# Optimization experiments

Hardware: AMD Instinct MI355X
Metric: run time of the kernel (lower is better)

The kernel has to match this reference:

```python
import jax, jax.numpy as jnp
import numpy as np

B, H, W, D, U = 32, 64, 64, 256, 512


def setup_inputs() -> dict:
    key = jax.random.key(0)
    k1, k2, k3, k4, k5 = jax.random.split(key, 5)
    he_in = np.sqrt(2.0 / D)
    he_u = np.sqrt(2.0 / U)
    return {
        "x": jax.random.normal(k1, (B, H, W, D), dtype=jnp.float32),
        "wax": jax.random.normal(k2, (D, U), dtype=jnp.float32) * he_in,
        "w0": jax.random.normal(k3, (U, U), dtype=jnp.float32) * he_u,
        "w1": jax.random.normal(k4, (U, U), dtype=jnp.float32) * he_u,
        "ba": jax.random.normal(k5, (1, U), dtype=jnp.float32) * 0.01,
    }


def reference(x, wax, w0, w1, ba):
    """2D MDRNN, direction (+1,+1), zero initial state, tanh activation.

    h[i,j] = tanh(x[i,j] @ wax + h[i-1,j] @ w0 + h[i,j-1] @ w1 + ba)
    (out-of-bound neighbors contribute zero, matching the original with
    zero initial state). Returns h at final position (H-1, W-1): (B, U).
    """
    b, h, w, d = x.shape
    u = wax.shape[1]
    # Precompute input contribution for the whole grid: (H, W, B, U)
    zx = jnp.einsum("bhwd,du->hwbu", x, wax) + ba

    def row_step(prev_row, zx_row):
        # prev_row: (W, B, U) = h[i-1, :]; zx_row: (W, B, U)
        pre = zx_row + jnp.einsum("wbu,uv->wbv", prev_row, w0)

        def col_step(h_left, pre_j):
            h_ij = jnp.tanh(pre_j + h_left @ w1)
            return h_ij, h_ij

        _, row = jax.lax.scan(col_step, jnp.zeros((b, u), x.dtype), pre)
        return row, None

    last_row, _ = jax.lax.scan(row_step, jnp.zeros((w, b, u), x.dtype), zx)
    return last_row[-1]  # (B, U)
```

## Files before the change

### kernel.cpp

```cpp
#include <hip/hip_runtime.h>
#include <stdint.h>

#define H_ 64
#define W_ 64
#define D_ 256
#define U_ 512
#define KREC 1024
#define CELL_ELT (32 * U_)

typedef __attribute__((ext_vector_type(8))) _Float16 half8;
typedef __attribute__((ext_vector_type(8))) unsigned short ushort8;
typedef __attribute__((ext_vector_type(4))) float f32x4;

__device__ __forceinline__ unsigned short f2h(float f) {
    _Float16 h = (_Float16)f;
    return __builtin_bit_cast(unsigned short, h);
}

__device__ __forceinline__ int swzo(int r, int o) {
    return o ^ (((r ^ (o >> 7)) & 7) << 4);
}

__device__ __forceinline__ void llc_load2(const int* p0, const int* p1, int& a, int& b) {
    asm volatile("global_load_dword %0, %2, off sc0 sc1\n\t"
                 "global_load_dword %1, %3, off sc0 sc1\n\t"
                 "s_waitcnt vmcnt(0)"
                 : "=v"(a), "=v"(b) : "v"(p0), "v"(p1) : "memory");
}

__global__ void prep_w(const float* __restrict__ w0,
                       const float* __restrict__ w1,
                       unsigned short* __restrict__ wcT2) {
    int n = blockIdx.x;
    for (int k = threadIdx.x; k < KREC; k += blockDim.x) {
        float v = (k < U_) ? w0[(size_t)k * U_ + n] : w1[(size_t)(k - U_) * U_ + n];
        wcT2[(size_t)n * KREC + k] = f2h(v);
    }
}

__global__ void prep_waxT(const float* __restrict__ wax,
                          unsigned short* __restrict__ waxT) {
    int n = blockIdx.x;
    for (int k = threadIdx.x; k < D_; k += blockDim.x)
        waxT[(size_t)n * D_ + k] = f2h(wax[(size_t)k * U_ + n]);
}

__global__ __launch_bounds__(256) void prep_z(
    const float* __restrict__ x,
    const unsigned short* __restrict__ waxT,
    const float* __restrict__ ba,
    float* __restrict__ zfb)
{
    __shared__ char xs[32 * 512];
    const int cell = blockIdx.x;
    const int t = threadIdx.x, lane = t & 63, wv = t >> 6;
    const int l15 = lane & 15, lh = lane >> 4;
    const int r = t >> 3, c8 = t & 7;

    {
        const float4* src = reinterpret_cast<const float4*>(
            x + (size_t)r * (H_ * W_ * D_) + (size_t)cell * D_ + c8 * 32);
        float4 f[8];
        #pragma unroll
        for (int q = 0; q < 8; ++q) f[q] = src[q];
        #pragma unroll
        for (int s = 0; s < 4; ++s) {
            float4 a = f[2 * s], b = f[2 * s + 1];
            ushort8 o;
            o[0] = f2h(a.x); o[1] = f2h(a.y); o[2] = f2h(a.z); o[3] = f2h(a.w);
            o[4] = f2h(b.x); o[5] = f2h(b.y); o[6] = f2h(b.z); o[7] = f2h(b.w);
            int ob = c8 * 64 + s * 16;
            *reinterpret_cast<ushort8*>(xs + r * 512 + swzo(r, ob)) = o;
        }
    }
    __syncthreads();

    f32x4 zero = {0.f, 0.f, 0.f, 0.f};
    f32x4 acc[2][8];
    #pragma unroll
    for (int m = 0; m < 2; ++m)
        #pragma unroll
        for (int n = 0; n < 8; ++n) acc[m][n] = zero;

    const char* ar0 = xs + l15 * 512;
    const char* ar1 = xs + (16 + l15) * 512;
    #pragma unroll
    for (int ks = 0; ks < 8; ++ks) {
        int ob = ks * 64 + lh * 16;
        int oo = swzo(l15, ob);
        half8 af0 = *reinterpret_cast<const half8*>(ar0 + oo);
        half8 af1 = *reinterpret_cast<const half8*>(ar1 + oo);
        #pragma unroll
        for (int ntg = 0; ntg < 8; ++ntg) {
            int col = wv * 128 + ntg * 16 + l15;
            half8 bf = *reinterpret_cast<const half8*>(waxT + (size_t)col * D_ + ks * 32 + lh * 8);
            acc[0][ntg] = __builtin_amdgcn_mfma_f32_16x16x32_f16(af0, bf, acc[0][ntg], 0, 0, 0);
            acc[1][ntg] = __builtin_amdgcn_mfma_f32_16x16x32_f16(af1, bf, acc[1][ntg], 0, 0, 0);
        }
    }

    #pragma unroll
    for (int s = 0; s < 4; ++s) {
        float* dst = zfb + (((size_t)cell * 16 + wv * 4 + s) * 64 + lane) * 16;
        #pragma unroll
        for (int mt = 0; mt < 2; ++mt)
            #pragma unroll
            for (int ntp = 0; ntp < 2; ++ntp) {
                float bav = ba[wv * 128 + s * 32 + ntp * 16 + l15];
                f32x4 o;
                o[0] = acc[mt][s * 2 + ntp][0] + bav;
                o[1] = acc[mt][s * 2 + ntp][1] + bav;
                o[2] = acc[mt][s * 2 + ntp][2] + bav;
                o[3] = acc[mt][s * 2 + ntp][3] + bav;
                *reinterpret_cast<f32x4*>(dst + mt * 8 + ntp * 4) = o;
            }
    }
}

__global__ __launch_bounds__(256, 1) void mdrnn_persistent(
    const unsigned short* __restrict__ wcT2,
    const float* __restrict__ zfb,
    unsigned short* __restrict__ hgrid,
    int* flags,
    float* __restrict__ out)
{
    __shared__ char smb[32 * 2048];
    __shared__ unsigned long long heps64[32 * 32];
    unsigned short* heps16 = reinterpret_cast<unsigned short*>(heps64);

    const int j  = (int)blockIdx.x >> 2;
    const int nc = (int)blockIdx.x & 3;
    const int t = threadIdx.x, lane = t & 63, wv = t >> 6;
    const int l15 = lane & 15, lh = lane >> 4;
    const int r = t >> 3, c8 = t & 7;
    const int gw = nc * 4 + wv;

    half8 breg[2][32];
    {
        const unsigned short* wb = wcT2 + (size_t)(nc * 128 + wv * 32 + l15) * KREC + lh * 8;
        #pragma unroll
        for (int nt = 0; nt < 2; ++nt)
            #pragma unroll
            for (int ks = 0; ks < 32; ++ks)
                breg[nt][ks] = *reinterpret_cast<const half8*>(wb + (size_t)nt * 16 * KREC + ks * 32);
    }

    #pragma clang loop unroll(disable)
    for (int i = 0; i < H_; ++i) {
        const int cell = i * W_ + j;

        const f32x4* zp = reinterpret_cast<const f32x4*>(
            zfb + (((size_t)cell * 16 + gw) * 64 + lane) * 16);
        f32x4 z0 = zp[0], z1 = zp[1], z2 = zp[2], z3 = zp[3];

        if (wv == 0 && (i > 0 || j > 0)) {
            const int* fu = (i > 0) ? flags + (cell - W_) : flags + (cell - 1);
            const int* fl = (j > 0) ? flags + (cell - 1) : flags + (cell - W_);
            for (;;) {
                int a, b;
                llc_load2(fu, fl, a, b);
                if (a >= 4 && b >= 4) break;
                __builtin_amdgcn_s_sleep(1);
            }
        }
        __syncthreads();

        if (i > 0) {
            const ushort8* us = reinterpret_cast<const ushort8*>(
                hgrid + (size_t)(cell - W_) * CELL_ELT + (size_t)r * U_ + c8 * 64);
            ushort8 ub[8];
            #pragma unroll
            for (int s = 0; s < 8; ++s) ub[s] = us[s];
            #pragma unroll
            for (int s = 0; s < 8; ++s) {
                int ob = c8 * 128 + s * 16;
                *reinterpret_cast<ushort8*>(smb + r * 2048 + swzo(r, ob)) = ub[s];
            }
        }
        if (j > 0) {
            const ushort8* ls = reinterpret_cast<const ushort8*>(
                hgrid + (size_t)(cell - 1) * CELL_ELT + (size_t)r * U_ + c8 * 64);
            ushort8 lb[8];
            #pragma unroll
            for (int s = 0; s < 8; ++s) lb[s] = ls[s];
            #pragma unroll
            for (int s = 0; s < 8; ++s) {
                int ob = 1024 + c8 * 128 + s * 16;
                *reinterpret_cast<ushort8*>(smb + r * 2048 + swzo(r, ob)) = lb[s];
            }
        }
        __syncthreads();

        f32x4 zero = {0.f, 0.f, 0.f, 0.f};
        f32x4 acc00 = zero, acc01 = zero, acc10 = zero, acc11 = zero;
        const char* ar0 = smb + l15 * 2048;
        const char* ar1 = smb + (16 + l15) * 2048;

#define MSTEP(ks)                                                                                \
        {                                                                                        \
            int ob = (ks) * 64 + lh * 16;                                                        \
            int oo = swzo(l15, ob);                                                              \
            half8 af0 = *reinterpret_cast<const half8*>(ar0 + oo);                               \
            half8 af1 = *reinterpret_cast<const half8*>(ar1 + oo);                               \
            acc00 = __builtin_amdgcn_mfma_f32_16x16x32_f16(af0, breg[0][(ks)], acc00, 0, 0, 0);  \
            acc01 = __builtin_amdgcn_mfma_f32_16x16x32_f16(af0, breg[1][(ks)], acc01, 0, 0, 0);  \
            acc10 = __builtin_amdgcn_mfma_f32_16x16x32_f16(af1, breg[0][(ks)], acc10, 0, 0, 0);  \
            acc11 = __builtin_amdgcn_mfma_f32_16x16x32_f16(af1, breg[1][(ks)], acc11, 0, 0, 0);  \
        }
        if (i > 0) {
            #pragma unroll
            for (int ks = 0; ks < 16; ++ks) MSTEP(ks)
        }
        if (j > 0) {
            #pragma unroll
            for (int ks = 16; ks < 32; ++ks) MSTEP(ks)
        }
#undef MSTEP

        const bool lastcell = (i == H_ - 1) && (j == W_ - 1);
        const int col0 = nc * 128 + wv * 32 + l15;
        #pragma unroll
        for (int mt = 0; mt < 2; ++mt) {
            f32x4 a0 = mt ? acc10 : acc00;
            f32x4 a1 = mt ? acc11 : acc01;
            f32x4 zq0 = mt ? z2 : z0;
            f32x4 zq1 = mt ? z3 : z1;
            #pragma unroll
            for (int rr = 0; rr < 4; ++rr) {
                int row = mt * 16 + lh * 4 + rr;
                float v0 = fminf(fmaxf(a0[rr] + zq0[rr], -15.f), 15.f);
                float v1 = fminf(fmaxf(a1[rr] + zq1[rr], -15.f), 15.f);
                float e0 = __expf(2.f * v0), e1 = __expf(2.f * v1);
                float th0 = (e0 - 1.f) / (e0 + 1.f);
                float th1 = (e1 - 1.f) / (e1 + 1.f);
                heps16[row * 128 + wv * 32 + l15]      = f2h(th0);
                heps16[row * 128 + wv * 32 + 16 + l15] = f2h(th1);
                if (lastcell) {
                    out[(size_t)row * U_ + col0]      = th0;
                    out[(size_t)row * U_ + col0 + 16] = th1;
                }
            }
        }
        __syncthreads();

        {
            const int erow = t >> 3, e = t & 7;
            unsigned long long* gq = reinterpret_cast<unsigned long long*>(
                hgrid + (size_t)cell * CELL_ELT + (size_t)erow * U_ + nc * 128);
            #pragma unroll
            for (int q = 0; q < 4; ++q) {
                unsigned long long v = heps64[erow * 32 + q * 8 + e];
                __hip_atomic_store(gq + q * 8 + e, v, __ATOMIC_RELAXED, __HIP_MEMORY_SCOPE_AGENT);
            }
        }

        asm volatile("s_waitcnt vmcnt(0)" ::: "memory");
        __syncthreads();
        if (t == 0)
            __hip_atomic_fetch_add(&flags[cell], 1, __ATOMIC_RELAXED, __HIP_MEMORY_SCOPE_AGENT);
    }
}

extern "C" void kernel_launch(void* const* d_in, const int* in_sizes, int n_in,
                              void* d_out, int out_size, void* d_ws, size_t ws_size,
                              hipStream_t stream) {
    const float* x   = (const float*)d_in[0];
    const float* wax = (const float*)d_in[1];
    const float* w0  = (const float*)d_in[2];
    const float* w1  = (const float*)d_in[3];
    const float* ba  = (const float*)d_in[4];
    float* out = (float*)d_out;

    char* w = (char*)d_ws;
    unsigned short* wcT2  = (unsigned short*)(w);
    unsigned short* waxT  = (unsigned short*)(w + (1u << 20));
    int*            flags = (int*)(w + (1u << 20) + (256u << 10));
    float*          zfb   = (float*)(w + (2u << 20));
    unsigned short* hgrid = (unsigned short*)(w + (2u << 20) + ((size_t)256 << 20));

    (void)hipMemsetAsync(flags, 0, (size_t)H_ * W_ * sizeof(int), stream);
    prep_w   <<<dim3(U_), dim3(256), 0, stream>>>(w0, w1, wcT2);
    prep_waxT<<<dim3(U_), dim3(256), 0, stream>>>(wax, waxT);
    prep_z   <<<dim3(H_ * W_), dim3(256), 0, stream>>>(x, waxT, ba, zfb);
    mdrnn_persistent<<<dim3(W_ * 4), dim3(256), 0, stream>>>(wcT2, zfb, hgrid, flags, out);
}
```

Baseline: 1.081 ms.

## Replace per-cell flag handshake with sentinel-value polling on hidden-state data

The per-cell completion flags are removed. The hidden-state grid is pre-filled with a 0x7F7F… sentinel pattern, which is NaN in fp16 and so can never be a tanh output. Each thread loads its slice of the up and left neighbour states directly with 64-bit atomic loads and re-polls only the words that still hold the sentinel. This drops the vmcnt wait, the extra barrier and the flag atomic on the producer side, plus the separate flag-poll round trip on the consumer side, which shortens the latency of each step along the wavefront critical path. In exchange, every launch now memsets the full 128 MB state grid, and consumers spin on data lines instead of a single flag.

```diff
diff --git a/kernel.cpp b/kernel.cpp
--- a/kernel.cpp
+++ b/kernel.cpp
@@ -19,13 +19,6 @@
 
 __device__ __forceinline__ int swzo(int r, int o) {
     return o ^ (((r ^ (o >> 7)) & 7) << 4);
-}
-
-__device__ __forceinline__ void llc_load2(const int* p0, const int* p1, int& a, int& b) {
-    asm volatile("global_load_dword %0, %2, off sc0 sc1\n\t"
-                 "global_load_dword %1, %3, off sc0 sc1\n\t"
-                 "s_waitcnt vmcnt(0)"
-                 : "=v"(a), "=v"(b) : "v"(p0), "v"(p1) : "memory");
 }
 
 __global__ void prep_w(const float* __restrict__ w0,
@@ -121,12 +114,13 @@
     const unsigned short* __restrict__ wcT2,
     const float* __restrict__ zfb,
     unsigned short* __restrict__ hgrid,
-    int* flags,
     float* __restrict__ out)
 {
     __shared__ char smb[32 * 2048];
     __shared__ unsigned long long heps64[32 * 32];
     unsigned short* heps16 = reinterpret_cast<unsigned short*>(heps64);
+
+    const unsigned long long P8 = 0x7F7F7F7F7F7F7F7FULL;
 
     const int j  = (int)blockIdx.x >> 2;
     const int nc = (int)blockIdx.x & 3;
@@ -153,40 +147,62 @@
             zfb + (((size_t)cell * 16 + gw) * 64 + lane) * 16);
         f32x4 z0 = zp[0], z1 = zp[1], z2 = zp[2], z3 = zp[3];
 
-        if (wv == 0 && (i > 0 || j > 0)) {
-            const int* fu = (i > 0) ? flags + (cell - W_) : flags + (cell - 1);
-            const int* fl = (j > 0) ? flags + (cell - 1) : flags + (cell - W_);
+        const bool nu = (i > 0), nl = (j > 0);
+        unsigned long long vu[16], vl[16];
+        const unsigned long long* ub64 = reinterpret_cast<const unsigned long long*>(
+            hgrid + (size_t)(cell - W_) * CELL_ELT + (size_t)r * U_ + c8 * 64);
+        const unsigned long long* lb64 = reinterpret_cast<const unsigned long long*>(
+            hgrid + (size_t)(cell - 1) * CELL_ELT + (size_t)r * U_ + c8 * 64);
+
+        if (nu) {
+            #pragma unroll
+            for (int q = 0; q < 16; ++q)
+                vu[q] = __hip_atomic_load(ub64 + q, __ATOMIC_RELAXED, __HIP_MEMORY_SCOPE_AGENT);
+        }
+        if (nl) {
+            #pragma unroll
+            for (int q = 0; q < 16; ++q)
+                vl[q] = __hip_atomic_load(lb64 + q, __ATOMIC_RELAXED, __HIP_MEMORY_SCOPE_AGENT);
+        }
+        if (nu || nl) {
             for (;;) {
-                int a, b;
-                llc_load2(fu, fl, a, b);
-                if (a >= 4 && b >= 4) break;
-                __builtin_amdgcn_s_sleep(1);
-            }
-        }
-        __syncthreads();
-
-        if (i > 0) {
-            const ushort8* us = reinterpret_cast<const ushort8*>(
-                hgrid + (size_t)(cell - W_) * CELL_ELT + (size_t)r * U_ + c8 * 64);
-            ushort8 ub[8];
-            #pragma unroll
-            for (int s = 0; s < 8; ++s) ub[s] = us[s];
-            #pragma unroll
-            for (int s = 0; s < 8; ++s) {
-                int ob = c8 * 128 + s * 16;
-                *reinterpret_cast<ushort8*>(smb + r * 2048 + swzo(r, ob)) = ub[s];
-            }
-        }
-        if (j > 0) {
-            const ushort8* ls = reinterpret_cast<const ushort8*>(
-                hgrid + (size_t)(cell - 1) * CELL_ELT + (size_t)r * U_ + c8 * 64);
-            ushort8 lb[8];
-            #pragma unroll
-            for (int s = 0; s < 8; ++s) lb[s] = ls[s];
-            #pragma unroll
-            for (int s = 0; s < 8; ++s) {
-                int ob = 1024 + c8 * 128 + s * 16;
-                *reinterpret_cast<ushort8*>(smb + r * 2048 + swzo(r, ob)) = lb[s];
+                bool stale = false;
+                if (nu) {
+                    #pragma unroll
+                    for (int q = 0; q < 16; ++q) stale |= (vu[q] == P8);
+                }
+                if (nl) {
+                    #pragma unroll
+                    for (int q = 0; q < 16; ++q) stale |= (vl[q] == P8);
+                }
+                if (!stale) break;
+                if (nu) {
+                    #pragma unroll
+                    for (int q = 0; q < 16; ++q)
+                        if (vu[q] == P8)
+                            vu[q] = __hip_atomic_load(ub64 + q, __ATOMIC_RELAXED, __HIP_MEMORY_SCOPE_AGENT);
+                }
+                if (nl) {
+                    #pragma unroll
+                    for (int q = 0; q < 16; ++q)
+                        if (vl[q] == P8)
+                            vl[q] = __hip_atomic_load(lb64 + q, __ATOMIC_RELAXED, __HIP_MEMORY_SCOPE_AGENT);
+                }
+            }
+        }
+
+        if (nu) {
+            #pragma unroll
+            for (int q = 0; q < 16; ++q) {
+                int ob = c8 * 128 + q * 8;
+                *reinterpret_cast<unsigned long long*>(smb + r * 2048 + swzo(r, ob)) = vu[q];
+            }
+        }
+        if (nl) {
+            #pragma unroll
+            for (int q = 0; q < 16; ++q) {
+                int ob = 1024 + c8 * 128 + q * 8;
+                *reinterpret_cast<unsigned long long*>(smb + r * 2048 + swzo(r, ob)) = vl[q];
             }
         }
         __syncthreads();
@@ -207,11 +223,11 @@
             acc10 = __builtin_amdgcn_mfma_f32_16x16x32_f16(af1, breg[0][(ks)], acc10, 0, 0, 0);  \
             acc11 = __builtin_amdgcn_mfma_f32_16x16x32_f16(af1, breg[1][(ks)], acc11, 0, 0, 0);  \
         }
-        if (i > 0) {
+        if (nu) {
             #pragma unroll
             for (int ks = 0; ks < 16; ++ks) MSTEP(ks)
         }
-        if (j > 0) {
+        if (nl) {
             #pragma unroll
             for (int ks = 16; ks < 32; ++ks) MSTEP(ks)
         }
@@ -253,11 +269,6 @@
                 __hip_atomic_store(gq + q * 8 + e, v, __ATOMIC_RELAXED, __HIP_MEMORY_SCOPE_AGENT);
             }
         }
-
-        asm volatile("s_waitcnt vmcnt(0)" ::: "memory");
-        __syncthreads();
-        if (t == 0)
-            __hip_atomic_fetch_add(&flags[cell], 1, __ATOMIC_RELAXED, __HIP_MEMORY_SCOPE_AGENT);
     }
 }
 
@@ -274,13 +285,12 @@
     char* w = (char*)d_ws;
     unsigned short* wcT2  = (unsigned short*)(w);
     unsigned short* waxT  = (unsigned short*)(w + (1u << 20));
-    int*            flags = (int*)(w + (1u << 20) + (256u << 10));
     float*          zfb   = (float*)(w + (2u << 20));
     unsigned short* hgrid = (unsigned short*)(w + (2u << 20) + ((size_t)256 << 20));
 
-    (void)hipMemsetAsync(flags, 0, (size_t)H_ * W_ * sizeof(int), stream);
+    (void)hipMemsetAsync(hgrid, 0x7F, (size_t)H_ * W_ * CELL_ELT * 2, stream);
     prep_w   <<<dim3(U_), dim3(256), 0, stream>>>(w0, w1, wcT2);
     prep_waxT<<<dim3(U_), dim3(256), 0, stream>>>(wax, waxT);
     prep_z   <<<dim3(H_ * W_), dim3(256), 0, stream>>>(x, waxT, ba, zfb);
-    mdrnn_persistent<<<dim3(W_ * 4), dim3(256), 0, stream>>>(wcT2, zfb, hgrid, flags, out);
-}
+    mdrnn_persistent<<<dim3(W_ * 4), dim3(256), 0, stream>>>(wcT2, zfb, hgrid, out);
+}
```

After: 1.641 ms. +51.7%, slower.
